# Performance work log

Measured on AMD Instinct MI355X. Metric: run time of the kernel, lower is better.

## Reference

```python
import jax, jax.numpy as jnp
import numpy as np

N = 50000          # num nodes
E = 800000         # num edges
H, C = 2, 64       # heads, per-head channels (hidden_dim=64)
IN_DIM = 128
EDGE_DIM = 32
NEG_SLOPE = 0.2


def setup_inputs() -> dict:
    key = jax.random.key(0)
    ks = jax.random.split(key, 20)
    s = 0.05
    inp = {
        'x': jax.random.normal(ks[0], (N, IN_DIM), jnp.float32),
        'edge_index': jax.random.randint(ks[1], (2, E), 0, N, jnp.int64),
        'edge_attr': jax.random.normal(ks[2], (E, EDGE_DIM), jnp.float32),
    }
    k = 3
    for l in range(3):
        inp[f'Wl{l}'] = jax.random.normal(ks[k], (IN_DIM, H * C), jnp.float32) * s; k += 1
        inp[f'Wr{l}'] = jax.random.normal(ks[k], (IN_DIM, H * C), jnp.float32) * s; k += 1
        inp[f'We{l}'] = jax.random.normal(ks[k], (EDGE_DIM, H * C), jnp.float32) * s; k += 1
        inp[f'att{l}'] = jax.random.normal(ks[k], (H, C), jnp.float32) * s; k += 1
        inp[f'b{l}'] = jnp.zeros((H * C,), jnp.float32)
    return inp


def gatv2_layer(x, src, dst, edge_attr, Wl, Wr, We, att, b):
    # PyG GATv2Conv (concat=True, share_weights=False):
    #   e_ij = att . LeakyReLU(Wl x_j + Wr x_i + We edge_ij)
    #   alpha = softmax_j over neighborhood of dst i; out_i = sum_j alpha_ij * (Wl x_j)
    xl = (x @ Wl).reshape(-1, H, C)              # [N,H,C] source transform
    xr = (x @ Wr).reshape(-1, H, C)              # [N,H,C] target transform
    ea = (edge_attr @ We).reshape(-1, H, C)      # [E,H,C]
    xj = xl[src]                                 # [E,H,C] gather source
    e = jax.nn.leaky_relu(xj + xr[dst] + ea, NEG_SLOPE)
    logits = jnp.einsum('ehc,hc->eh', e, att)    # [E,H]
    # segment softmax over dst neighborhoods
    m = jax.ops.segment_max(logits, dst, num_segments=N)  # [N,H]
    m = jnp.where(jnp.isfinite(m), m, 0.0)
    ex = jnp.exp(logits - m[dst])
    denom = jax.ops.segment_sum(ex, dst, num_segments=N)  # [N,H]
    alpha = ex / (denom[dst] + 1e-16)            # [E,H]
    out = jax.ops.segment_sum(alpha[:, :, None] * xj, dst, num_segments=N)  # [N,H,C]
    return out.reshape(-1, H * C) + b


def reference(x, edge_index, edge_attr,
              Wl0, Wr0, We0, att0, b0,
              Wl1, Wr1, We1, att1, b1,
              Wl2, Wr2, We2, att2, b2):
    src, dst = edge_index[0], edge_index[1]
    h = gatv2_layer(x, src, dst, edge_attr, Wl0, Wr0, We0, att0, b0)
    h = jax.nn.relu(h)
    h = gatv2_layer(h, src, dst, edge_attr, Wl1, Wr1, We1, att1, b1)
    h = jax.nn.relu(h)
    h = gatv2_layer(h, src, dst, edge_attr, Wl2, Wr2, We2, att2, b2)
    return h
```

## Files before the change

### kernel.cpp

```cpp
#include <hip/hip_runtime.h>

typedef unsigned int u32;
typedef unsigned short u16;
typedef __attribute__((ext_vector_type(8))) short bf16x8;
typedef __attribute__((ext_vector_type(4))) float f32x4;

__device__ __forceinline__ u16 f2b(float f){
  u32 x = __float_as_uint(f);
  u32 r = (x + 0x7fffu + ((x >> 16) & 1u)) >> 16;
  return (u16)r;
}
__device__ __forceinline__ float b2f(u16 h){ return __uint_as_float((u32)h << 16); }
__device__ __forceinline__ float bl(u32 u){ return __uint_as_float(u << 16); }
__device__ __forceinline__ float bh(u32 u){ return __uint_as_float(u & 0xffff0000u); }


__global__ void k_detect(const u32* __restrict__ ei, int n, u32* __restrict__ flag){
  int t = blockIdx.x * blockDim.x + threadIdx.x;
  u32 v = 0;
  if (t < n) v = ei[2 * t + 1];
  unsigned long long b = __ballot(v != 0u);
  if ((threadIdx.x & 63) == 0 && b) atomicOr(flag, 1u);
}

__global__ void k_convhist(const int* __restrict__ ei, int* __restrict__ src, int* __restrict__ dst,
                           int* __restrict__ deg, int E, const u32* __restrict__ flag){
  int e = blockIdx.x * blockDim.x + threadIdx.x;
  if (e >= E) return;
  bool is64 = (*flag == 0u);
  int s, d;
  if (is64){ s = ei[2 * e]; d = ei[2 * (E + e)]; }
  else     { s = ei[e];     d = ei[E + e]; }
  src[e] = s; dst[e] = d;
  atomicAdd(&deg[d], 1);
}

__global__ __launch_bounds__(256) void k_scan1(const int* __restrict__ deg, int* __restrict__ bsum, int n,
                                               int* __restrict__ ssrc, int* __restrict__ sdst,
                                               u16* __restrict__ ea2s_pad, int E){
  int b = blockIdx.x, t = threadIdx.x, lane = t & 63, wv = t >> 6;
  if (b == 0){
    if (t < 64){ ssrc[E + t] = 0; sdst[E + t] = 0; }
    ((uint4*)ea2s_pad)[t] = make_uint4(0, 0, 0, 0);
  }
  int i0 = b * 1024 + t * 4;
  int4 v = make_int4(0,0,0,0);
  if (i0 + 3 < n) v = *(const int4*)(deg + i0);
  else { if (i0 < n) v.x = deg[i0]; if (i0+1 < n) v.y = deg[i0+1]; if (i0+2 < n) v.z = deg[i0+2]; }
  int s = v.x + v.y + v.z + v.w;
  #pragma unroll
  for (int off = 1; off < 64; off <<= 1) s += __shfl_xor(s, off);
  __shared__ int ws[4];
  if (lane == 0) ws[wv] = s;
  __syncthreads();
  if (t == 0) bsum[b] = ws[0] + ws[1] + ws[2] + ws[3];
}

__global__ __launch_bounds__(1024) void k_scan2(int* __restrict__ bsum, int nb, int* __restrict__ segN){
  int t = threadIdx.x, lane = t & 63, w = t >> 6;
  int v = (t < nb) ? bsum[t] : 0;
  int x = v;
  #pragma unroll
  for (int off = 1; off < 64; off <<= 1){
    int y = __shfl_up(x, off);
    if (lane >= off) x += y;
  }
  __shared__ int wsum[16];
  if (lane == 63) wsum[w] = x;
  __syncthreads();
  if (w == 0 && lane < 16){
    int sv = wsum[lane];
    #pragma unroll
    for (int off = 1; off < 16; off <<= 1){
      int y = __shfl_up(sv, off);
      if (lane >= off) sv += y;
    }
    wsum[lane] = sv;
  }
  __syncthreads();
  int woff = (w > 0) ? wsum[w - 1] : 0;
  if (t < nb) bsum[t] = woff + x - v;
  if (t == 0) *segN = wsum[15];
}

__global__ __launch_bounds__(256) void k_scan3(const int* __restrict__ deg, const int* __restrict__ bsum,
                                               int* __restrict__ seg, int n){
  int b = blockIdx.x, t = threadIdx.x, lane = t & 63, wv = t >> 6;
  int i0 = b * 1024 + t * 4;
  int4 v = make_int4(0,0,0,0);
  if (i0 + 3 < n) v = *(const int4*)(deg + i0);
  else { if (i0 < n) v.x = deg[i0]; if (i0+1 < n) v.y = deg[i0+1]; if (i0+2 < n) v.z = deg[i0+2]; }
  int s = v.x + v.y + v.z + v.w;
  int x = s;
  #pragma unroll
  for (int off = 1; off < 64; off <<= 1){
    int y = __shfl_up(x, off);
    if (lane >= off) x += y;
  }
  __shared__ int ws[4];
  if (lane == 63) ws[wv] = x;
  __syncthreads();
  int woff = 0;
  #pragma unroll
  for (int k = 0; k < 4; k++) if (k < wv) woff += ws[k];
  int base = bsum[b] + woff + (x - s);
  if (i0 < n)     seg[i0]     = base;
  if (i0+1 < n)   seg[i0+1]   = base + v.x;
  if (i0+2 < n)   seg[i0+2]   = base + v.x + v.y;
  if (i0+3 < n)   seg[i0+3]   = base + v.x + v.y + v.z;
}

__global__ void k_scatter(const int* __restrict__ src, const int* __restrict__ dst,
                          const int* __restrict__ seg, int* __restrict__ cur,
                          int* __restrict__ ssrc, int* __restrict__ sdst,
                          int* __restrict__ seid, int E){
  int e = blockIdx.x * blockDim.x + threadIdx.x;
  if (e >= E) return;
  int d = dst[e];
  int pos = seg[d] + atomicAdd(&cur[d], 1);
  ssrc[pos] = src[e];
  sdst[pos] = d;
  seid[pos] = e;
}

__global__ void k_sortb(const int* __restrict__ seid, const float* __restrict__ eattr,
                        u16* __restrict__ ea2s, int E){
  int t = blockIdx.x * blockDim.x + threadIdx.x;
  int e = t >> 3, j = t & 7;
  if (e >= E) return;
  int eid = seid[e];
  float4 v = *(const float4*)(eattr + (size_t)eid * 32 + j * 4);
  u32 p0 = (u32)f2b(v.x) | ((u32)f2b(v.y) << 16);
  u32 p1 = (u32)f2b(v.z) | ((u32)f2b(v.w) << 16);
  *(uint2*)(ea2s + (size_t)e * 32 + j * 4) = make_uint2(p0, p1);
}

__global__ __launch_bounds__(256) void k_prepw(
    const float* __restrict__ W0, const float* __restrict__ W1, const float* __restrict__ W2,
    const float* __restrict__ W3, const float* __restrict__ W4, const float* __restrict__ W5,
    u16* __restrict__ WtH, u16* __restrict__ WtL)
{
  int mat = blockIdx.z;
  const float* W = (mat == 0) ? W0 : (mat == 1) ? W1 : (mat == 2) ? W2 :
                   (mat == 3) ? W3 : (mat == 4) ? W4 : W5;
  __shared__ float tile[32][33];
  int kt = blockIdx.x * 32, ct = blockIdx.y * 32;
  int tr = threadIdx.x & 31, ti = threadIdx.x >> 5;
  #pragma unroll
  for (int j = 0; j < 4; j++){
    int kk = ti + 8 * j;
    tile[kk][tr] = W[(size_t)(kt + kk) * 128 + ct + tr];
  }
  __syncthreads();
  #pragma unroll
  for (int j = 0; j < 4; j++){
    int cc = ti + 8 * j;
    float v = tile[tr][cc];
    u16 hi = f2b(v);
    u16 lo = f2b(v - b2f(hi));
    size_t o = (size_t)mat * 16384 + (size_t)(ct + cc) * 128 + kt + tr;
    WtH[o] = hi;
    WtL[o] = lo;
  }
}

__global__ __launch_bounds__(256) void k_gemm2(
    const float* __restrict__ A,
    const u16* __restrict__ WtH, const u16* __restrict__ WtL,
    u16* __restrict__ xlb, u16* __restrict__ xrb, int nrows)
{
  __shared__ u16 sAH[64][32], sAL[64][32];
  __shared__ u16 sWH[128][32], sWL[128][32];
  int t = threadIdx.x, wv = t >> 6, lane = t & 63;
  int col = lane & 15, kg = lane >> 4;
  int r0 = blockIdx.x * 64;
  int mat = blockIdx.y;
  const u16* WHb = WtH + (size_t)mat * 16384;
  const u16* WLb = WtL + (size_t)mat * 16384;

  f32x4 acc[4][2];
  #pragma unroll
  for (int m = 0; m < 4; m++)
    #pragma unroll
    for (int n = 0; n < 2; n++)
      acc[m][n] = (f32x4){0.f, 0.f, 0.f, 0.f};

  int ar = t >> 2, ak = (t & 3) << 3;
  int wc = t >> 1, wk = (t & 1) << 4;

  for (int kh = 0; kh < 4; kh++){
    __syncthreads();
    {
      int gr = r0 + ar;
      const float* ap = A + (size_t)gr * 128 + kh * 32 + ak;
      float4 va = {0,0,0,0}, vb = {0,0,0,0};
      if (gr < nrows){ va = *(const float4*)ap; vb = *(const float4*)(ap + 4); }
      float fv[8] = { va.x, va.y, va.z, va.w, vb.x, vb.y, vb.z, vb.w };
      u32 hp[4], lp[4];
      #pragma unroll
      for (int i = 0; i < 4; i++){
        u16 h0 = f2b(fv[2*i]),   h1 = f2b(fv[2*i+1]);
        u16 l0 = f2b(fv[2*i]   - b2f(h0));
        u16 l1 = f2b(fv[2*i+1] - b2f(h1));
        hp[i] = (u32)h0 | ((u32)h1 << 16);
        lp[i] = (u32)l0 | ((u32)l1 << 16);
      }
      *(uint4*)&sAH[ar][ak] = make_uint4(hp[0], hp[1], hp[2], hp[3]);
      *(uint4*)&sAL[ar][ak] = make_uint4(lp[0], lp[1], lp[2], lp[3]);
    }
    {
      const u16* gh = WHb + (size_t)wc * 128 + kh * 32 + wk;
      const u16* gl = WLb + (size_t)wc * 128 + kh * 32 + wk;
      uint4 h0 = *(const uint4*)gh, h1 = *(const uint4*)(gh + 8);
      uint4 l0 = *(const uint4*)gl, l1 = *(const uint4*)(gl + 8);
      *(uint4*)&sWH[wc][wk]     = h0; *(uint4*)&sWH[wc][wk + 8] = h1;
      *(uint4*)&sWL[wc][wk]     = l0; *(uint4*)&sWL[wc][wk + 8] = l1;
    }
    __syncthreads();
    bf16x8 bhi0 = *(const bf16x8*)&sWH[wv*32 + col]     [kg*8];
    bf16x8 bhi1 = *(const bf16x8*)&sWH[wv*32 + 16 + col][kg*8];
    bf16x8 blo0 = *(const bf16x8*)&sWL[wv*32 + col]     [kg*8];
    bf16x8 blo1 = *(const bf16x8*)&sWL[wv*32 + 16 + col][kg*8];
    #pragma unroll
    for (int m = 0; m < 4; m++){
      bf16x8 ahv = *(const bf16x8*)&sAH[m*16 + col][kg*8];
      bf16x8 alv = *(const bf16x8*)&sAL[m*16 + col][kg*8];
      acc[m][0] = __builtin_amdgcn_mfma_f32_16x16x32_bf16(ahv, bhi0, acc[m][0], 0, 0, 0);
      acc[m][0] = __builtin_amdgcn_mfma_f32_16x16x32_bf16(alv, bhi0, acc[m][0], 0, 0, 0);
      acc[m][0] = __builtin_amdgcn_mfma_f32_16x16x32_bf16(ahv, blo0, acc[m][0], 0, 0, 0);
      acc[m][1] = __builtin_amdgcn_mfma_f32_16x16x32_bf16(ahv, bhi1, acc[m][1], 0, 0, 0);
      acc[m][1] = __builtin_amdgcn_mfma_f32_16x16x32_bf16(alv, bhi1, acc[m][1], 0, 0, 0);
      acc[m][1] = __builtin_amdgcn_mfma_f32_16x16x32_bf16(ahv, blo1, acc[m][1], 0, 0, 0);
    }
  }
  u16* ob = mat ? xrb : xlb;
  #pragma unroll
  for (int m = 0; m < 4; m++){
    #pragma unroll
    for (int n = 0; n < 2; n++){
      #pragma unroll
      for (int r = 0; r < 4; r++){
        int row = r0 + m*16 + kg*4 + r;
        int c   = wv*32 + n*16 + col;
        if (row < nrows) ob[(size_t)row * 128 + c] = f2b(acc[m][n][r]);
      }
    }
  }
}

__global__ __launch_bounds__(256) void k_edge(
    const int* __restrict__ ssrc, const int* __restrict__ sdst,
    const u16* __restrict__ ea2s,
    const u16* __restrict__ xlb, const u16* __restrict__ xrb,
    const float* __restrict__ We, const float* __restrict__ att,
    float2* __restrict__ pr2, int ntiles, int E)
{
  __shared__ float sD[4][16][132];
  int wv = threadIdx.x >> 6, lane = threadIdx.x & 63;
  int col = lane & 15, kg = lane >> 4;
  int er = lane >> 2, q = lane & 3;

  bf16x8 bw[8];
  #pragma unroll
  for (int c = 0; c < 8; c++)
    #pragma unroll
    for (int j = 0; j < 8; j++)
      bw[c][j] = (short)f2b(We[(kg * 8 + j) * 128 + c * 16 + col]);
  u32 attp[16];
  #pragma unroll
  for (int i = 0; i < 16; i++)
    attp[i] = (u32)f2b(att[q * 32 + 2*i]) | ((u32)f2b(att[q * 32 + 2*i + 1]) << 16);

  int nw = gridDim.x * 4;
  int bid = blockIdx.x;
  if ((gridDim.x & 7) == 0){
    int cpx = gridDim.x >> 3;
    bid = (bid & 7) * cpx + (bid >> 3);
  }
  int t = bid * 4 + wv;
  if (t >= ntiles) return;

  int e0 = t * 16;
  int p = e0 + er;
  bf16x8 aA = *(const bf16x8*)(ea2s + (size_t)(e0 + col) * 32 + kg * 8);
  int snA = ssrc[p], dnA = sdst[p];
  const u16* xjA = xlb + (size_t)snA * 128 + q * 32;
  uint4 jA0 = ((const uint4*)xjA)[0], jA1 = ((const uint4*)xjA)[1],
        jA2 = ((const uint4*)xjA)[2], jA3 = ((const uint4*)xjA)[3];

  int tB = t + nw;
  int tBc = (tB < ntiles) ? tB : t;
  int eB = tBc * 16;
  int pB = eB + er;
  bf16x8 aB = *(const bf16x8*)(ea2s + (size_t)(eB + col) * 32 + kg * 8);
  int snB = ssrc[pB], dnB = sdst[pB];
  const u16* xjB = xlb + (size_t)snB * 128 + q * 32;
  uint4 jB0 = ((const uint4*)xjB)[0], jB1 = ((const uint4*)xjB)[1],
        jB2 = ((const uint4*)xjB)[2], jB3 = ((const uint4*)xjB)[3];

  while (true){
    const u16* xip = xrb + (size_t)dnA * 128 + q * 32;
    uint4 i0 = ((const uint4*)xip)[0], i1 = ((const uint4*)xip)[1],
          i2 = ((const uint4*)xip)[2], i3 = ((const uint4*)xip)[3];

    int tC = t + 2 * nw;
    int tCc = (tC < ntiles) ? tC : t;
    int eC = tCc * 16;
    int pC = eC + er;
    bf16x8 aC = *(const bf16x8*)(ea2s + (size_t)(eC + col) * 32 + kg * 8);
    int snC = ssrc[pC], dnC = sdst[pC];
    const u16* xjC = xlb + (size_t)snC * 128 + q * 32;
    uint4 jC0 = ((const uint4*)xjC)[0], jC1 = ((const uint4*)xjC)[1],
          jC2 = ((const uint4*)xjC)[2], jC3 = ((const uint4*)xjC)[3];

    #pragma unroll
    for (int c = 0; c < 8; c++){
      f32x4 d = __builtin_amdgcn_mfma_f32_16x16x32_bf16(aA, bw[c], (f32x4){0.f,0.f,0.f,0.f}, 0, 0, 0);
      #pragma unroll
      for (int r = 0; r < 4; r++)
        sD[wv][kg * 4 + r][c * 16 + col] = d[r];
    }

    const float* drow = &sD[wv][er][q * 32];
    float acc = 0.f;
#define EPK(KO, JQ, IQ) { \
    float4 d0 = *(const float4*)(drow + KO*8); \
    float4 d1 = *(const float4*)(drow + KO*8 + 4); \
    float v; u32 jw, iw, aw; \
    jw = JQ.x; iw = IQ.x; aw = attp[KO*4+0]; \
    v = d0.x + bl(jw) + bl(iw); v = fmaxf(v, 0.2f*v); acc = fmaf(v, bl(aw), acc); \
    v = d0.y + bh(jw) + bh(iw); v = fmaxf(v, 0.2f*v); acc = fmaf(v, bh(aw), acc); \
    jw = JQ.y; iw = IQ.y; aw = attp[KO*4+1]; \
    v = d0.z + bl(jw) + bl(iw); v = fmaxf(v, 0.2f*v); acc = fmaf(v, bl(aw), acc); \
    v = d0.w + bh(jw) + bh(iw); v = fmaxf(v, 0.2f*v); acc = fmaf(v, bh(aw), acc); \
    jw = JQ.z; iw = IQ.z; aw = attp[KO*4+2]; \
    v = d1.x + bl(jw) + bl(iw); v = fmaxf(v, 0.2f*v); acc = fmaf(v, bl(aw), acc); \
    v = d1.y + bh(jw) + bh(iw); v = fmaxf(v, 0.2f*v); acc = fmaf(v, bh(aw), acc); \
    jw = JQ.w; iw = IQ.w; aw = attp[KO*4+3]; \
    v = d1.z + bl(jw) + bl(iw); v = fmaxf(v, 0.2f*v); acc = fmaf(v, bl(aw), acc); \
    v = d1.w + bh(jw) + bh(iw); v = fmaxf(v, 0.2f*v); acc = fmaf(v, bh(aw), acc); }
    EPK(0, jA0, i0) EPK(1, jA1, i1) EPK(2, jA2, i2) EPK(3, jA3, i3)
#undef EPK
    acc += __shfl_xor(acc, 1);
    float other = __shfl_xor(acc, 2);
    if (q == 0 && p < E){
      pr2[p] = make_float2(__expf(fminf(acc, 80.f)), __expf(fminf(other, 80.f)));
    }
    int t2 = t + nw;
    if (t2 >= ntiles) break;
    t = t2; p = pB;
    aA = aB; dnA = dnB;
    jA0 = jB0; jA1 = jB1; jA2 = jB2; jA3 = jB3;
    aB = aC; dnB = dnC; pB = pC;
    jB0 = jC0; jB1 = jC1; jB2 = jC2; jB3 = jC3;
  }
}

template<int RELU>
__global__ __launch_bounds__(256) void k_seg2(
    const int* __restrict__ seg, const int* __restrict__ ssrc,
    const float2* __restrict__ pr2,
    const u16* __restrict__ xlb, const float* __restrict__ bias,
    float* __restrict__ out, int N)
{
  int wid  = blockIdx.x * 4 + (threadIdx.x >> 6);
  int lane = threadIdx.x & 63;
  if (wid >= N) return;
  int eg = lane >> 4, cb = lane & 15, c0 = cb * 8;
  int hsel = cb >> 3;

  int p0 = seg[wid], p1 = seg[wid + 1];
  float s = 0.f;
  float o0 = 0.f, o1 = 0.f, o2 = 0.f, o3 = 0.f, o4 = 0.f, o5 = 0.f, o6 = 0.f, o7 = 0.f;

  if (p0 < p1){
#define LDB(PP, QV, XV) { \
    int ii = PP + eg; ii = (ii < p1) ? ii : (p1 - 1); \
    int sn = ssrc[ii]; \
    QV = pr2[ii]; \
    XV = *(const uint4*)(xlb + (size_t)sn * 128 + c0); }
    int p = p0;
    float2 qa; uint4 xa;
    LDB(p, qa, xa)
    int pBb = p + 4; int pBc = (pBb < p1) ? pBb : p;
    float2 qb; uint4 xb;
    LDB(pBc, qb, xb)
    while (true){
      int pCb = p + 8; int pCc = (pCb < p1) ? pCb : p;
      float2 qc; uint4 xc;
      LDB(pCc, qc, xc)
      float e = hsel ? qa.y : qa.x;
      if (p + eg >= p1) e = 0.f;
      s += e;
      o0 = fmaf(e, bl(xa.x), o0); o1 = fmaf(e, bh(xa.x), o1);
      o2 = fmaf(e, bl(xa.y), o2); o3 = fmaf(e, bh(xa.y), o3);
      o4 = fmaf(e, bl(xa.z), o4); o5 = fmaf(e, bh(xa.z), o5);
      o6 = fmaf(e, bl(xa.w), o6); o7 = fmaf(e, bh(xa.w), o7);
      if (p + 4 >= p1) break;
      p += 4;
      qa = qb; xa = xb;
      qb = qc; xb = xc;
    }
#undef LDB
  }
  s  += __shfl_xor(s, 16);  s  += __shfl_xor(s, 32);
  o0 += __shfl_xor(o0, 16); o0 += __shfl_xor(o0, 32);
  o1 += __shfl_xor(o1, 16); o1 += __shfl_xor(o1, 32);
  o2 += __shfl_xor(o2, 16); o2 += __shfl_xor(o2, 32);
  o3 += __shfl_xor(o3, 16); o3 += __shfl_xor(o3, 32);
  o4 += __shfl_xor(o4, 16); o4 += __shfl_xor(o4, 32);
  o5 += __shfl_xor(o5, 16); o5 += __shfl_xor(o5, 32);
  o6 += __shfl_xor(o6, 16); o6 += __shfl_xor(o6, 32);
  o7 += __shfl_xor(o7, 16); o7 += __shfl_xor(o7, 32);

  if (eg == 0){
    float inv = 1.0f / (s + 1e-16f);
    float4 b0 = *(const float4*)(bias + c0);
    float4 b1 = *(const float4*)(bias + c0 + 4);
    float r0 = fmaf(o0, inv, b0.x), r1 = fmaf(o1, inv, b0.y);
    float r2 = fmaf(o2, inv, b0.z), r3 = fmaf(o3, inv, b0.w);
    float r4 = fmaf(o4, inv, b1.x), r5 = fmaf(o5, inv, b1.y);
    float r6 = fmaf(o6, inv, b1.z), r7 = fmaf(o7, inv, b1.w);
    if (RELU){
      r0 = fmaxf(r0, 0.f); r1 = fmaxf(r1, 0.f); r2 = fmaxf(r2, 0.f); r3 = fmaxf(r3, 0.f);
      r4 = fmaxf(r4, 0.f); r5 = fmaxf(r5, 0.f); r6 = fmaxf(r6, 0.f); r7 = fmaxf(r7, 0.f);
    }
    *(float4*)(out + (size_t)wid * 128 + c0)     = make_float4(r0, r1, r2, r3);
    *(float4*)(out + (size_t)wid * 128 + c0 + 4) = make_float4(r4, r5, r6, r7);
  }
}

extern "C" void kernel_launch(void* const* d_in, const int* in_sizes, int n_in,
                              void* d_out, int out_size, void* d_ws, size_t ws_size,
                              hipStream_t stream)
{
  const float* x     = (const float*)d_in[0];
  const int*   ei    = (const int*)  d_in[1];
  const float* eattr = (const float*)d_in[2];
  const float* Wp[3][5];
  for (int l = 0; l < 3; l++)
    for (int j = 0; j < 5; j++)
      Wp[l][j] = (const float*)d_in[3 + l * 5 + j];

  int N = in_sizes[0] / 128;
  int E = in_sizes[2] / 32;

  char* w = (char*)d_ws;
  auto alloc = [&](size_t bytes) -> char* {
    char* p = w; w += (bytes + 255) & ~(size_t)255; return p;
  };
  float* xr   = (float*)alloc((size_t)N * 128 * 4);
  u16*   xlb  = (u16*)  alloc((size_t)N * 128 * 2);
  u16*   xrb  = (u16*)  alloc((size_t)N * 128 * 2);
  u16*   ea2s = (u16*)  alloc((size_t)(E + 64) * 32 * 2);
  float2* prb = (float2*)alloc((size_t)E * 8);
  u16*   WtH  = (u16*)  alloc((size_t)6 * 16384 * 2);
  u16*   WtL  = (u16*)  alloc((size_t)6 * 16384 * 2);
  int* srcA   = (int*)alloc((size_t)E * 4);
  int* dstA   = (int*)alloc((size_t)E * 4);
  int* ssrc   = (int*)alloc((size_t)(E + 64) * 4);
  int* sdst   = (int*)alloc((size_t)(E + 64) * 4);
  int* seid   = (int*)alloc((size_t)E * 4);
  int* seg    = (int*)alloc((size_t)(N + 1) * 4);
  int* bsum   = (int*)alloc(1024 * 4);
  char* zbase = alloc((size_t)N * 4);      int* deg  = (int*)zbase;
  char* zcur  = alloc((size_t)N * 4);      int* cur  = (int*)zcur;
  char* zflag = alloc(256);                u32* flag = (u32*)zflag;
  size_t zspan = (size_t)(zflag + 256 - zbase);

  hipMemsetAsync(zbase, 0, zspan, stream);

  int ndet = (E < 16384) ? E : 16384;
  k_detect<<<(ndet + 255) / 256, 256, 0, stream>>>((const u32*)ei, ndet, flag);
  int gE = (E + 255) / 256;
  k_convhist<<<gE, 256, 0, stream>>>(ei, srcA, dstA, deg, E, flag);
  int nb = (N + 1023) / 1024;
  k_scan1<<<nb, 256, 0, stream>>>(deg, bsum, N, ssrc, sdst, ea2s + (size_t)E * 32, E);
  k_scan2<<<1, 1024, 0, stream>>>(bsum, nb, seg + N);
  k_scan3<<<nb, 256, 0, stream>>>(deg, bsum, seg, N);
  k_scatter<<<gE, 256, 0, stream>>>(srcA, dstA, seg, cur, ssrc, sdst, seid, E);
  k_sortb<<<(E * 8 + 255) / 256, 256, 0, stream>>>(seid, eattr, ea2s, E);
  dim3 gp(4, 4, 6);
  k_prepw<<<gp, 256, 0, stream>>>(Wp[0][0], Wp[0][1], Wp[1][0], Wp[1][1], Wp[2][0], Wp[2][1], WtH, WtL);

  int gS = (N + 3) / 4;
  int ntiles = (E + 15) / 16;
  int gEdge = (ntiles + 3) / 4; if (gEdge > 2048) gEdge = 2048;
  dim3 gG2((N + 63) / 64, 2);

  const float* hin = x;
  for (int l = 0; l < 3; l++){
    k_gemm2<<<gG2, 256, 0, stream>>>(hin, WtH + (size_t)l * 2 * 16384, WtL + (size_t)l * 2 * 16384, xlb, xrb, N);
    k_edge<<<gEdge, 256, 0, stream>>>(ssrc, sdst, ea2s, xlb, xrb, Wp[l][2], Wp[l][3], prb, ntiles, E);
    float* outp = (l == 2) ? (float*)d_out : xr;
    if (l == 2) k_seg2<0><<<gS, 256, 0, stream>>>(seg, ssrc, prb, xlb, Wp[l][4], outp, N);
    else        k_seg2<1><<<gS, 256, 0, stream>>>(seg, ssrc, prb, xlb, Wp[l][4], outp, N);
    hin = xr;
  }
}
```

Before: 471.1 us.

## Compute both Wl and Wr projections in one 512-thread GEMM block sharing A tile

The GEMM kernel now uses 512-thread blocks in which four waves compute the Wl projection and four compute the Wr projection. The input rows are loaded and split into bf16 hi/lo once per block instead of once per output matrix, which halves the reads and conversion work on the activation matrix. The cost is more shared memory per block, since both weight tiles are staged, and larger blocks. Separately, the XCD-aware block-index remapping in the edge kernel is removed in favour of plain linear block ordering.

After: 466.4 us. No clear change (-1.0%).

```diff
diff --git a/kernel.cpp b/kernel.cpp
--- a/kernel.cpp
+++ b/kernel.cpp
@@ -164,19 +164,17 @@
   }
 }
 
-__global__ __launch_bounds__(256) void k_gemm2(
+__global__ __launch_bounds__(512) void k_gemm2(
     const float* __restrict__ A,
     const u16* __restrict__ WtH, const u16* __restrict__ WtL,
     u16* __restrict__ xlb, u16* __restrict__ xrb, int nrows)
 {
   __shared__ u16 sAH[64][32], sAL[64][32];
-  __shared__ u16 sWH[128][32], sWL[128][32];
+  __shared__ u16 sWH[256][32], sWL[256][32];
   int t = threadIdx.x, wv = t >> 6, lane = t & 63;
   int col = lane & 15, kg = lane >> 4;
+  int mat = wv >> 2, cq = wv & 3;
   int r0 = blockIdx.x * 64;
-  int mat = blockIdx.y;
-  const u16* WHb = WtH + (size_t)mat * 16384;
-  const u16* WLb = WtL + (size_t)mat * 16384;
 
   f32x4 acc[4][2];
   #pragma unroll
@@ -185,42 +183,37 @@
     for (int n = 0; n < 2; n++)
       acc[m][n] = (f32x4){0.f, 0.f, 0.f, 0.f};
 
-  int ar = t >> 2, ak = (t & 3) << 3;
-  int wc = t >> 1, wk = (t & 1) << 4;
+  int ar = t >> 3, ak = (t & 7) << 2;
+  int wmt = t >> 8, wtt = t & 255;
+  int wc = wtt >> 1, wk = (wtt & 1) << 4;
 
   for (int kh = 0; kh < 4; kh++){
     __syncthreads();
     {
       int gr = r0 + ar;
       const float* ap = A + (size_t)gr * 128 + kh * 32 + ak;
-      float4 va = {0,0,0,0}, vb = {0,0,0,0};
-      if (gr < nrows){ va = *(const float4*)ap; vb = *(const float4*)(ap + 4); }
-      float fv[8] = { va.x, va.y, va.z, va.w, vb.x, vb.y, vb.z, vb.w };
-      u32 hp[4], lp[4];
-      #pragma unroll
-      for (int i = 0; i < 4; i++){
-        u16 h0 = f2b(fv[2*i]),   h1 = f2b(fv[2*i+1]);
-        u16 l0 = f2b(fv[2*i]   - b2f(h0));
-        u16 l1 = f2b(fv[2*i+1] - b2f(h1));
-        hp[i] = (u32)h0 | ((u32)h1 << 16);
-        lp[i] = (u32)l0 | ((u32)l1 << 16);
-      }
-      *(uint4*)&sAH[ar][ak] = make_uint4(hp[0], hp[1], hp[2], hp[3]);
-      *(uint4*)&sAL[ar][ak] = make_uint4(lp[0], lp[1], lp[2], lp[3]);
+      float4 va = {0,0,0,0};
+      if (gr < nrows) va = *(const float4*)ap;
+      u16 h0 = f2b(va.x), h1 = f2b(va.y), h2 = f2b(va.z), h3 = f2b(va.w);
+      u16 l0 = f2b(va.x - b2f(h0)), l1 = f2b(va.y - b2f(h1));
+      u16 l2 = f2b(va.z - b2f(h2)), l3 = f2b(va.w - b2f(h3));
+      *(uint2*)&sAH[ar][ak] = make_uint2((u32)h0 | ((u32)h1 << 16), (u32)h2 | ((u32)h3 << 16));
+      *(uint2*)&sAL[ar][ak] = make_uint2((u32)l0 | ((u32)l1 << 16), (u32)l2 | ((u32)l3 << 16));
     }
     {
-      const u16* gh = WHb + (size_t)wc * 128 + kh * 32 + wk;
-      const u16* gl = WLb + (size_t)wc * 128 + kh * 32 + wk;
+      const u16* gh = WtH + (size_t)wmt * 16384 + (size_t)wc * 128 + kh * 32 + wk;
+      const u16* gl = WtL + (size_t)wmt * 16384 + (size_t)wc * 128 + kh * 32 + wk;
       uint4 h0 = *(const uint4*)gh, h1 = *(const uint4*)(gh + 8);
       uint4 l0 = *(const uint4*)gl, l1 = *(const uint4*)(gl + 8);
-      *(uint4*)&sWH[wc][wk]     = h0; *(uint4*)&sWH[wc][wk + 8] = h1;
-      *(uint4*)&sWL[wc][wk]     = l0; *(uint4*)&sWL[wc][wk + 8] = l1;
+      *(uint4*)&sWH[wmt * 128 + wc][wk]     = h0; *(uint4*)&sWH[wmt * 128 + wc][wk + 8] = h1;
+      *(uint4*)&sWL[wmt * 128 + wc][wk]     = l0; *(uint4*)&sWL[wmt * 128 + wc][wk + 8] = l1;
     }
     __syncthreads();
-    bf16x8 bhi0 = *(const bf16x8*)&sWH[wv*32 + col]     [kg*8];
-    bf16x8 bhi1 = *(const bf16x8*)&sWH[wv*32 + 16 + col][kg*8];
-    bf16x8 blo0 = *(const bf16x8*)&sWL[wv*32 + col]     [kg*8];
-    bf16x8 blo1 = *(const bf16x8*)&sWL[wv*32 + 16 + col][kg*8];
+    int wb = mat * 128 + cq * 32;
+    bf16x8 bhi0 = *(const bf16x8*)&sWH[wb + col]     [kg*8];
+    bf16x8 bhi1 = *(const bf16x8*)&sWH[wb + 16 + col][kg*8];
+    bf16x8 blo0 = *(const bf16x8*)&sWL[wb + col]     [kg*8];
+    bf16x8 blo1 = *(const bf16x8*)&sWL[wb + 16 + col][kg*8];
     #pragma unroll
     for (int m = 0; m < 4; m++){
       bf16x8 ahv = *(const bf16x8*)&sAH[m*16 + col][kg*8];
@@ -241,7 +234,7 @@
       #pragma unroll
       for (int r = 0; r < 4; r++){
         int row = r0 + m*16 + kg*4 + r;
-        int c   = wv*32 + n*16 + col;
+        int c   = cq*32 + n*16 + col;
         if (row < nrows) ob[(size_t)row * 128 + c] = f2b(acc[m][n][r]);
       }
     }
@@ -272,12 +265,7 @@
     attp[i] = (u32)f2b(att[q * 32 + 2*i]) | ((u32)f2b(att[q * 32 + 2*i + 1]) << 16);
 
   int nw = gridDim.x * 4;
-  int bid = blockIdx.x;
-  if ((gridDim.x & 7) == 0){
-    int cpx = gridDim.x >> 3;
-    bid = (bid & 7) * cpx + (bid >> 3);
-  }
-  int t = bid * 4 + wv;
+  int t = blockIdx.x * 4 + wv;
   if (t >= ntiles) return;
 
   int e0 = t * 16;
@@ -486,11 +474,11 @@
   int gS = (N + 3) / 4;
   int ntiles = (E + 15) / 16;
   int gEdge = (ntiles + 3) / 4; if (gEdge > 2048) gEdge = 2048;
-  dim3 gG2((N + 63) / 64, 2);
+  int gG2 = (N + 63) / 64;
 
   const float* hin = x;
   for (int l = 0; l < 3; l++){
-    k_gemm2<<<gG2, 256, 0, stream>>>(hin, WtH + (size_t)l * 2 * 16384, WtL + (size_t)l * 2 * 16384, xlb, xrb, N);
+    k_gemm2<<<gG2, 512, 0, stream>>>(hin, WtH + (size_t)l * 2 * 16384, WtL + (size_t)l * 2 * 16384, xlb, xrb, N);
     k_edge<<<gEdge, 256, 0, stream>>>(ssrc, sdst, ea2s, xlb, xrb, Wp[l][2], Wp[l][3], prb, ntiles, E);
     float* outp = (l == 2) ? (float*)d_out : xr;
     if (l == 2) k_seg2<0><<<gS, 256, 0, stream>>>(seg, ssrc, prb, xlb, Wp[l][4], outp, N);
```
